# Optimization experiments

Measured on AMD Instinct MI355X. Metric: run time of the kernel, lower is better.

## Reference

```python
import jax, jax.numpy as jnp
import numpy as np

DECAY = 0.5  # fixed decay constant from the module


def _decay_scan(x):
    """Linear recurrence y_i = DECAY * y_{i-1} + x_i along axis 1, as a
    log-depth associative scan. x: [B, S, H]."""
    a = jnp.full_like(x, DECAY)

    def combine(c1, c2):
        a1, b1 = c1
        a2, b2 = c2
        return (a1 * a2, a2 * b1 + b2)

    _, y = jax.lax.associative_scan(combine, (a, x), axis=1)
    return y


def setup_inputs() -> dict:
    key = jax.random.key(0)
    batch = jax.random.normal(key, (16, 2048, 1024), dtype=jnp.float32)
    return {"batch": batch}


def reference(batch) -> jnp.ndarray:
    # Forward-in-time decay aggregate: fwd[i] = sum_{k<=i} d^{i-k} x[k]
    fwd = _decay_scan(batch)
    # Backward-in-time decay aggregate: bwd[i] = sum_{k>=i} d^{k-i} x[k]
    bwd = jnp.flip(_decay_scan(jnp.flip(batch, axis=1)), axis=1)
    S = batch.shape[1]
    k = jnp.arange(S, dtype=batch.dtype)
    # closed-form geometric sum: n[i] = sum_{j=0}^{i} d^j = (1 - d^{i+1}) / (1 - d)
    n_fwd = (1.0 - DECAY ** (k + 1.0)) / (1.0 - DECAY)
    norm = n_fwd + n_fwd[::-1]  # [S]; note word i is counted in both passes
    return (fwd + bwd) / norm[None, :, None]
```

## Files before the change

### kernel.cpp

```cpp
#include <hip/hip_runtime.h>


constexpr int B = 16;
constexpr int S = 2048;
constexpr int H = 1024;
constexpr int HV = H / 4;
constexpr int C = 128;
constexpr int W = 16;
constexpr int NT = C / W;
constexpr int K = 12;
constexpr int THREADS = 128;
constexpr int NH = HV / THREADS;
constexpr int NCH = S / C;

typedef float v4f __attribute__((ext_vector_type(4)));

__global__ __launch_bounds__(THREADS, 1) void decay_kernel(
    const v4f* __restrict__ x, v4f* __restrict__ out) {
    const int chunk = blockIdx.x / NH;
    const int hsel = blockIdx.x % NH;
    const int b = blockIdx.y;
    const int s0 = chunk * C;

    const size_t colBase = (size_t)b * S * HV + (size_t)(hsel * THREADS) +
                           threadIdx.x;
    const v4f* __restrict__ xp = x + colBase;
    v4f* __restrict__ op = out + colBase;

    v4f xb[3][W];
    v4f hv[K];

#pragma unroll
    for (int r = 0; r < K; ++r) {
        const int s = s0 - K + r;
        const int sc = s < 0 ? 0 : s;
        hv[r] = xp[(size_t)sc * HV];
    }
#pragma unroll
    for (int r = 0; r < W; ++r) xb[0][r] = xp[(size_t)(s0 + r) * HV];
#pragma unroll
    for (int r = 0; r < W; ++r) xb[1][r] = xp[(size_t)(s0 + W + r) * HV];

    v4f facc = (v4f)0.0f;
    if (chunk > 0) {
#pragma unroll
        for (int r = 0; r < K; ++r) facc = 0.5f * facc + hv[r];
    }

    const bool interior = (s0 >= 32) && (s0 + C <= S - 32);
    const bool lastChunk = (chunk == NCH - 1);

#pragma unroll
    for (int n = 0; n < NT; ++n) {
        if (n + 2 < NT) {
#pragma unroll
            for (int r = 0; r < W; ++r)
                xb[(n + 2) % 3][r] = xp[(size_t)(s0 + (n + 2) * W + r) * HV];
        } else if (n + 2 == NT) {
#pragma unroll
            for (int r = 0; r < K; ++r) {
                const int s = s0 + C + r;
                const int sc = s > S - 1 ? S - 1 : s;
                xb[(n + 2) % 3][r] = xp[(size_t)sc * HV];
            }
        }

        const v4f fprev = facc;
#pragma unroll
        for (int r = 0; r < W; ++r) {
            facc = 0.5f * facc + xb[n % 3][r];
            xb[n % 3][r] = facc;
        }

        if (n == NT - 1) {
            if (lastChunk) {
#pragma unroll
                for (int r = 0; r < K; ++r) xb[(n + 1) % 3][r] = (v4f)0.0f;
            }
        }

        v4f bacc = (v4f)0.0f;
#pragma unroll
        for (int j = K - 1; j >= 0; --j)
            bacc = 0.5f * bacc + xb[(n + 1) % 3][j];
#pragma unroll
        for (int r = W - 1; r >= 0; --r) {
            const v4f f = xb[n % 3][r];
            const v4f fm1 = (r > 0) ? xb[n % 3][r - 1] : fprev;
            const v4f xt = f - 0.5f * fm1;
            bacc = 0.5f * bacc + xt;
            const int i = s0 + n * W + r;
            float rn = 0.25f;
            if (!interior) {
                rn = 1.0f / (4.0f - exp2f((float)(-i)) -
                             exp2f((float)(i - (S - 1))));
            }
            __builtin_nontemporal_store((f + bacc) * rn, &op[(size_t)i * HV]);
        }
    }
}

extern "C" void kernel_launch(void* const* d_in, const int* in_sizes, int n_in,
                              void* d_out, int out_size, void* d_ws,
                              size_t ws_size, hipStream_t stream) {
    const v4f* x = (const v4f*)d_in[0];
    v4f* out = (v4f*)d_out;
    dim3 grid(NCH * NH, B);
    decay_kernel<<<grid, THREADS, 0, stream>>>(x, out);
}
```

Baseline: 238.1 us.

## Use smaller chunks with full-row blocks and XCD-aware block swizzle

Shrinks the sequence chunk from 128 to 32 rows and drops the three-buffer software pipeline in favour of loading the whole chunk plus left and right halos into registers at once. Each block now covers all 256 vector columns with 256 threads. Blocks are swizzled so that consecutive chunks of a batch land on the same XCD, and launch bounds allow 4 blocks per CU to raise occupancy. The cost is halo re-read overhead: 24 extra rows per 32, versus 24 per 128 before, which adds global read traffic in exchange for more parallelism and memory-level concurrency.

```diff
diff --git a/kernel.cpp b/kernel.cpp
--- a/kernel.cpp
+++ b/kernel.cpp
@@ -5,98 +5,77 @@
 constexpr int S = 2048;
 constexpr int H = 1024;
 constexpr int HV = H / 4;
-constexpr int C = 128;
-constexpr int W = 16;
-constexpr int NT = C / W;
+constexpr int C = 32;
 constexpr int K = 12;
-constexpr int THREADS = 128;
-constexpr int NH = HV / THREADS;
+constexpr int THREADS = 256;
 constexpr int NCH = S / C;
+constexpr int NBLK = NCH * B;
+constexpr int NXCD = 8;
 
 typedef float v4f __attribute__((ext_vector_type(4)));
 
-__global__ __launch_bounds__(THREADS, 1) void decay_kernel(
+__global__ __launch_bounds__(THREADS, 4) void decay_kernel(
     const v4f* __restrict__ x, v4f* __restrict__ out) {
-    const int chunk = blockIdx.x / NH;
-    const int hsel = blockIdx.x % NH;
-    const int b = blockIdx.y;
+    const int bid = blockIdx.x;
+    const int swz = (bid % NXCD) * (NBLK / NXCD) + bid / NXCD;
+    const int chunk = swz % NCH;
+    const int b = swz / NCH;
     const int s0 = chunk * C;
 
-    const size_t colBase = (size_t)b * S * HV + (size_t)(hsel * THREADS) +
-                           threadIdx.x;
+    const size_t colBase = (size_t)b * S * HV + threadIdx.x;
     const v4f* __restrict__ xp = x + colBase;
     v4f* __restrict__ op = out + colBase;
 
-    v4f xb[3][W];
-    v4f hv[K];
-
+    v4f xl[K], xa[C], xr[K];
 #pragma unroll
     for (int r = 0; r < K; ++r) {
         const int s = s0 - K + r;
-        const int sc = s < 0 ? 0 : s;
-        hv[r] = xp[(size_t)sc * HV];
+        xl[r] = xp[(size_t)(s < 0 ? 0 : s) * HV];
     }
 #pragma unroll
-    for (int r = 0; r < W; ++r) xb[0][r] = xp[(size_t)(s0 + r) * HV];
+    for (int r = 0; r < C; ++r) xa[r] = xp[(size_t)(s0 + r) * HV];
 #pragma unroll
-    for (int r = 0; r < W; ++r) xb[1][r] = xp[(size_t)(s0 + W + r) * HV];
+    for (int r = 0; r < K; ++r) {
+        const int s = s0 + C + r;
+        xr[r] = xp[(size_t)(s > S - 1 ? S - 1 : s) * HV];
+    }
+    if (chunk == 0) {
+#pragma unroll
+        for (int r = 0; r < K; ++r) xl[r] = (v4f)0.0f;
+    }
+    if (chunk == NCH - 1) {
+#pragma unroll
+        for (int r = 0; r < K; ++r) xr[r] = (v4f)0.0f;
+    }
 
     v4f facc = (v4f)0.0f;
-    if (chunk > 0) {
 #pragma unroll
-        for (int r = 0; r < K; ++r) facc = 0.5f * facc + hv[r];
+    for (int r = 0; r < K; ++r) facc = 0.5f * facc + xl[r];
+    const v4f fm1 = facc;
+#pragma unroll
+    for (int r = 0; r < C; ++r) {
+        facc = 0.5f * facc + xa[r];
+        xa[r] = facc;
     }
 
+    v4f bacc = (v4f)0.0f;
+#pragma unroll
+    for (int r = K - 1; r >= 0; --r) bacc = 0.5f * bacc + xr[r];
+
     const bool interior = (s0 >= 32) && (s0 + C <= S - 32);
-    const bool lastChunk = (chunk == NCH - 1);
-
 #pragma unroll
-    for (int n = 0; n < NT; ++n) {
-        if (n + 2 < NT) {
-#pragma unroll
-            for (int r = 0; r < W; ++r)
-                xb[(n + 2) % 3][r] = xp[(size_t)(s0 + (n + 2) * W + r) * HV];
-        } else if (n + 2 == NT) {
-#pragma unroll
-            for (int r = 0; r < K; ++r) {
-                const int s = s0 + C + r;
-                const int sc = s > S - 1 ? S - 1 : s;
-                xb[(n + 2) % 3][r] = xp[(size_t)sc * HV];
-            }
+    for (int r = C - 1; r >= 0; --r) {
+        const v4f f = xa[r];
+        const v4f fp = (r > 0) ? xa[r - 1] : fm1;
+        const v4f xt = f - 0.5f * fp;
+        bacc = 0.5f * bacc + xt;
+        const int i = s0 + r;
+        float rn = 0.25f;
+        if (!interior) {
+            rn = 1.0f / (4.0f - exp2f((float)(-i)) -
+                         exp2f((float)(i - (S - 1))));
         }
-
-        const v4f fprev = facc;
-#pragma unroll
-        for (int r = 0; r < W; ++r) {
-            facc = 0.5f * facc + xb[n % 3][r];
-            xb[n % 3][r] = facc;
-        }
-
-        if (n == NT - 1) {
-            if (lastChunk) {
-#pragma unroll
-                for (int r = 0; r < K; ++r) xb[(n + 1) % 3][r] = (v4f)0.0f;
-            }
-        }
-
-        v4f bacc = (v4f)0.0f;
-#pragma unroll
-        for (int j = K - 1; j >= 0; --j)
-            bacc = 0.5f * bacc + xb[(n + 1) % 3][j];
-#pragma unroll
-        for (int r = W - 1; r >= 0; --r) {
-            const v4f f = xb[n % 3][r];
-            const v4f fm1 = (r > 0) ? xb[n % 3][r - 1] : fprev;
-            const v4f xt = f - 0.5f * fm1;
-            bacc = 0.5f * bacc + xt;
-            const int i = s0 + n * W + r;
-            float rn = 0.25f;
-            if (!interior) {
-                rn = 1.0f / (4.0f - exp2f((float)(-i)) -
-                             exp2f((float)(i - (S - 1))));
-            }
-            __builtin_nontemporal_store((f + bacc) * rn, &op[(size_t)i * HV]);
-        }
+        __builtin_nontemporal_store((f + bacc) * rn, &op[(size_t)i * HV]);
     }
 }
 
@@ -105,6 +84,5 @@
                               size_t ws_size, hipStream_t stream) {
     const v4f* x = (const v4f*)d_in[0];
     v4f* out = (v4f*)d_out;
-    dim3 grid(NCH * NH, B);
-    decay_kernel<<<grid, THREADS, 0, stream>>>(x, out);
+    decay_kernel<<<dim3(NBLK), THREADS, 0, stream>>>(x, out);
 }
```

Measured after the change: 301.6 us. +26.6%, slower.

## Stream inputs through LDS with direct global-to-LDS loads and 4-deep ring buffer

Applied to the files above, without the earlier changes.

Replaces register-staged row loads with global_load_lds async copies into a 4-slot LDS ring buffer, so the next tiles can be fetched while the current tile is scanned. Tile width drops from 16 to 8 rows, and explicit vmcnt waits manage the pipeline. Blocks are also remapped through a swizzled 1D grid to spread batches and chunks across XCDs. The aim is to hide load latency at occupancy of one block per CU. It adds LDS traffic and manual waitcnt synchronisation that depend on exact counting of in-flight loads, and there is no barrier between waves, which is only safe if each wave reads just the LDS data it loaded itself.

```diff
diff --git a/kernel.cpp b/kernel.cpp
--- a/kernel.cpp
+++ b/kernel.cpp
@@ -1,102 +1,138 @@
 #include <hip/hip_runtime.h>
+#include <stdint.h>
 
 
 constexpr int B = 16;
 constexpr int S = 2048;
-constexpr int H = 1024;
-constexpr int HV = H / 4;
+constexpr int HV = 256;
 constexpr int C = 128;
-constexpr int W = 16;
+constexpr int W = 8;
 constexpr int NT = C / W;
 constexpr int K = 12;
 constexpr int THREADS = 128;
-constexpr int NH = HV / THREADS;
-constexpr int NCH = S / C;
+constexpr int BH = 128;
+constexpr int NBUF = 4;
+constexpr int NCHUNK = S / C;
+constexpr int NBLK = B * NCHUNK * (HV / BH);
 
 typedef float v4f __attribute__((ext_vector_type(4)));
 
+__device__ __forceinline__ void gload16(const v4f* g, v4f* l) {
+    __builtin_amdgcn_global_load_lds(
+        (const __attribute__((address_space(1))) uint32_t*)g,
+        (__attribute__((address_space(3))) uint32_t*)l, 16, 0, 0);
+}
+
+template <int PH>
+__device__ __forceinline__ void body(int n, int s0, int slim, bool edge,
+                                     const v4f* __restrict__ xp,
+                                     v4f* __restrict__ op, int tid, int wv,
+                                     v4f (*lds)[W][BH], v4f& facc) {
+    constexpr int bcur = PH & 3;
+    constexpr int bnx1 = (PH + 1) & 3;
+    constexpr int bnx2 = (PH + 2) & 3;
+    constexpr int bprf = (PH + 3) & 3;
+
+    if (n + 3 <= NT + 1) {
+#pragma unroll
+        for (int r = 0; r < W; ++r) {
+            int srow = s0 + (n + 3) * W + r;
+            srow = srow > S - 1 ? S - 1 : srow;
+            gload16(xp + (size_t)srow * HV, &lds[bprf][r][wv * 64]);
+        }
+    }
+    asm volatile("s_waitcnt vmcnt(8)" ::: "memory");
+
+    const v4f fprev = facc;
+    v4f f[W];
+    v4f fa = facc;
+#pragma unroll
+    for (int r = 0; r < W; ++r) {
+        fa = 0.5f * fa + lds[bcur][r][tid];
+        f[r] = fa;
+    }
+    facc = fa;
+
+    v4f bacc = (v4f)0.0f;
+#pragma unroll
+    for (int j = K - 1; j >= 0; --j) {
+        v4f t = (j < W) ? lds[bnx1][j][tid] : lds[bnx2][j - W][tid];
+        if ((n + 1) * W + j >= slim) t = (v4f)0.0f;
+        bacc = 0.5f * bacc + t;
+    }
+
+#pragma unroll
+    for (int r = W - 1; r >= 0; --r) {
+        const v4f fr = f[r];
+        const v4f fm = r ? f[r - 1] : fprev;
+        bacc = 0.5f * bacc + (fr - 0.5f * fm);
+        const int i = s0 + n * W + r;
+        float rn = 0.25f;
+        if (edge)
+            rn = 1.0f / (4.0f - exp2f((float)(-i)) -
+                         exp2f((float)(i - (S - 1))));
+        __builtin_nontemporal_store((fr + bacc) * rn, op + (size_t)i * HV);
+    }
+}
+
 __global__ __launch_bounds__(THREADS, 1) void decay_kernel(
     const v4f* __restrict__ x, v4f* __restrict__ out) {
-    const int chunk = blockIdx.x / NH;
-    const int hsel = blockIdx.x % NH;
-    const int b = blockIdx.y;
-    const int s0 = chunk * C;
+    __shared__ v4f lds[NBUF][W][BH];
 
-    const size_t colBase = (size_t)b * S * HV + (size_t)(hsel * THREADS) +
-                           threadIdx.x;
+    const int bid = blockIdx.x;
+    const int swz = (bid & 7) * (NBLK / 8) + (bid >> 3);
+    const int h = swz & 1;
+    const int cc = (swz >> 1) & (NCHUNK - 1);
+    const int b = swz >> 5;
+    const int s0 = cc * C;
+    const int slim = S - s0;
+    const bool edge = (cc == 0) | (cc == NCHUNK - 1);
+
+    const int tid = threadIdx.x;
+    const int wv = tid >> 6;
+
+    const size_t colBase = (size_t)b * S * HV + (size_t)(h * BH) + tid;
     const v4f* __restrict__ xp = x + colBase;
     v4f* __restrict__ op = out + colBase;
 
-    v4f xb[3][W];
-    v4f hv[K];
-
 #pragma unroll
-    for (int r = 0; r < K; ++r) {
-        const int s = s0 - K + r;
-        const int sc = s < 0 ? 0 : s;
-        hv[r] = xp[(size_t)sc * HV];
+    for (int r = 4; r < W; ++r) {
+        int srow = s0 - 2 * W + r;
+        srow = srow < 0 ? 0 : srow;
+        gload16(xp + (size_t)srow * HV, &lds[2][r][wv * 64]);
     }
 #pragma unroll
-    for (int r = 0; r < W; ++r) xb[0][r] = xp[(size_t)(s0 + r) * HV];
+    for (int r = 0; r < W; ++r) {
+        int srow = s0 - W + r;
+        srow = srow < 0 ? 0 : srow;
+        gload16(xp + (size_t)srow * HV, &lds[3][r][wv * 64]);
+    }
 #pragma unroll
-    for (int r = 0; r < W; ++r) xb[1][r] = xp[(size_t)(s0 + W + r) * HV];
+    for (int r = 0; r < W; ++r)
+        gload16(xp + (size_t)(s0 + r) * HV, &lds[0][r][wv * 64]);
+#pragma unroll
+    for (int r = 0; r < W; ++r)
+        gload16(xp + (size_t)(s0 + W + r) * HV, &lds[1][r][wv * 64]);
+
+    asm volatile("s_waitcnt vmcnt(16)" ::: "memory");
 
     v4f facc = (v4f)0.0f;
-    if (chunk > 0) {
+    if (s0 > 0) {
 #pragma unroll
-        for (int r = 0; r < K; ++r) facc = 0.5f * facc + hv[r];
+        for (int r = 4; r < W; ++r) facc = 0.5f * facc + lds[2][r][tid];
+#pragma unroll
+        for (int r = 0; r < W; ++r) facc = 0.5f * facc + lds[3][r][tid];
+        asm volatile("s_waitcnt lgkmcnt(0)" ::: "memory");
     }
+#pragma unroll
+    for (int r = 0; r < W; ++r)
+        gload16(xp + (size_t)(s0 + 2 * W + r) * HV, &lds[2][r][wv * 64]);
 
-    const bool interior = (s0 >= 32) && (s0 + C <= S - 32);
-    const bool lastChunk = (chunk == NCH - 1);
-
-#pragma unroll
-    for (int n = 0; n < NT; ++n) {
-        if (n + 2 < NT) {
-#pragma unroll
-            for (int r = 0; r < W; ++r)
-                xb[(n + 2) % 3][r] = xp[(size_t)(s0 + (n + 2) * W + r) * HV];
-        } else if (n + 2 == NT) {
-#pragma unroll
-            for (int r = 0; r < K; ++r) {
-                const int s = s0 + C + r;
-                const int sc = s > S - 1 ? S - 1 : s;
-                xb[(n + 2) % 3][r] = xp[(size_t)sc * HV];
-            }
-        }
-
-        const v4f fprev = facc;
-#pragma unroll
-        for (int r = 0; r < W; ++r) {
-            facc = 0.5f * facc + xb[n % 3][r];
-            xb[n % 3][r] = facc;
-        }
-
-        if (n == NT - 1) {
-            if (lastChunk) {
-#pragma unroll
-                for (int r = 0; r < K; ++r) xb[(n + 1) % 3][r] = (v4f)0.0f;
-            }
-        }
-
-        v4f bacc = (v4f)0.0f;
-#pragma unroll
-        for (int j = K - 1; j >= 0; --j)
-            bacc = 0.5f * bacc + xb[(n + 1) % 3][j];
-#pragma unroll
-        for (int r = W - 1; r >= 0; --r) {
-            const v4f f = xb[n % 3][r];
-            const v4f fm1 = (r > 0) ? xb[n % 3][r - 1] : fprev;
-            const v4f xt = f - 0.5f * fm1;
-            bacc = 0.5f * bacc + xt;
-            const int i = s0 + n * W + r;
-            float rn = 0.25f;
-            if (!interior) {
-                rn = 1.0f / (4.0f - exp2f((float)(-i)) -
-                             exp2f((float)(i - (S - 1))));
-            }
-            __builtin_nontemporal_store((f + bacc) * rn, &op[(size_t)i * HV]);
-        }
+    for (int t = 0; t < NT; t += 4) {
+        body<0>(t + 0, s0, slim, edge, xp, op, tid, wv, lds, facc);
+        body<1>(t + 1, s0, slim, edge, xp, op, tid, wv, lds, facc);
+        body<2>(t + 2, s0, slim, edge, xp, op, tid, wv, lds, facc);
+        body<3>(t + 3, s0, slim, edge, xp, op, tid, wv, lds, facc);
     }
 }
 
@@ -105,6 +141,5 @@
                               size_t ws_size, hipStream_t stream) {
     const v4f* x = (const v4f*)d_in[0];
     v4f* out = (v4f*)d_out;
-    dim3 grid(NCH * NH, B);
-    decay_kernel<<<grid, THREADS, 0, stream>>>(x, out);
+    decay_kernel<<<dim3(NBLK), THREADS, 0, stream>>>(x, out);
 }
```

Result: no change. 240.6 us (+1.0%).
